# Optimization experiments

Hardware: AMD Instinct MI355X
Metric: run time of the kernel (lower is better)

## Reference

```python
import jax, jax.numpy as jnp
import numpy as np

HIDDEN = 64


def _lstm_cell(x, h, c, W_ih, W_hh, b_ih, b_hh):
    # gates: [B, 4*H], torch LSTMCell order: i, f, g, o
    gates = x @ W_ih.T + h @ W_hh.T + b_ih + b_hh
    i, f, g, o = jnp.split(gates, 4, axis=-1)
    i = jax.nn.sigmoid(i)
    f = jax.nn.sigmoid(f)
    g = jnp.tanh(g)
    o = jax.nn.sigmoid(o)
    c_new = f * c + i * g
    h_new = o * jnp.tanh(c_new)
    return h_new, c_new


def setup_inputs() -> dict:
    key = jax.random.key(0)
    ks = jax.random.split(key, 12)
    B, L, H = 1024, 512, HIDDEN
    k = 1.0 / np.sqrt(H)  # torch LSTMCell/Linear init scale
    u = lambda kk, shape: jax.random.uniform(kk, shape, jnp.float32, -k, k)
    return {
        "y": jax.random.normal(ks[0], (B, L), jnp.float32),
        "W_ih1": u(ks[1], (4 * H, 1)),
        "W_hh1": u(ks[2], (4 * H, H)),
        "b_ih1": u(ks[3], (4 * H,)),
        "b_hh1": u(ks[4], (4 * H,)),
        "W_ih2": u(ks[5], (4 * H, H)),
        "W_hh2": u(ks[6], (4 * H, H)),
        "b_ih2": u(ks[7], (4 * H,)),
        "b_hh2": u(ks[8], (4 * H,)),
        "W_lin": u(ks[9], (1, H)),
        "b_lin": u(ks[10], (1,)),
        "future_preds": 0,
    }


def reference(y, W_ih1, W_hh1, b_ih1, b_hh1, W_ih2, W_hh2, b_ih2, b_hh2,
              W_lin, b_lin, future_preds):
    B = y.shape[0]
    H = HIDDEN
    zeros = jnp.zeros((B, H), jnp.float32)

    def step(carry, x_t):
        h1, c1, h2, c2 = carry
        h1, c1 = _lstm_cell(x_t, h1, c1, W_ih1, W_hh1, b_ih1, b_hh1)
        h2, c2 = _lstm_cell(h1, h2, c2, W_ih2, W_hh2, b_ih2, b_hh2)
        out = h2 @ W_lin.T + b_lin  # [B, 1]
        return (h1, c1, h2, c2), out

    xs = y.T[:, :, None]  # [L, B, 1]
    carry, outs = jax.lax.scan(step, (zeros, zeros, zeros, zeros), xs)
    outputs = outs[:, :, 0].T  # [B, L]

    if future_preds > 0:
        def fstep(fc, _):
            h1, c1, h2, c2, out = fc
            h1, c1 = _lstm_cell(out, h1, c1, W_ih1, W_hh1, b_ih1, b_hh1)
            h2, c2 = _lstm_cell(h1, h2, c2, W_ih2, W_hh2, b_ih2, b_hh2)
            out = h2 @ W_lin.T + b_lin
            return (h1, c1, h2, c2, out), out
        last_out = outs[-1]  # [B, 1]
        _, fouts = jax.lax.scan(fstep, (*carry, last_out), None,
                                length=future_preds)
        outputs = jnp.concatenate([outputs, fouts[:, :, 0].T], axis=1)
    return outputs
```

## Files before the change

### kernel.cpp

```cpp
#include <hip/hip_runtime.h>
#include <math.h>

#define LSEQ 512

typedef float  f32x4  __attribute__((ext_vector_type(4)));
typedef short  bf16x8 __attribute__((ext_vector_type(8)));

union Frag { uint32_t u[4]; bf16x8 h; };

__device__ __forceinline__ float frcp(float x) { return __builtin_amdgcn_rcpf(x); }
__device__ __forceinline__ float sigm(float x) { return frcp(1.0f + exp2f(-1.442695041f * x)); }
__device__ __forceinline__ float tanh_fast(float x) {
    float e = exp2f(2.885390082f * x);
    return 1.0f - 2.0f * frcp(e + 1.0f);
}

__device__ __forceinline__ uint32_t pack_hi_u(uint32_t b0, uint32_t b1) {
    return __builtin_amdgcn_perm(b1, b0, 0x07060302u);
}

__device__ __forceinline__ void load_wfrag(const float* __restrict__ W, int sl, int nn, int g4,
                                           Frag fh[4][2], Frag fl[4][2]) {
#pragma unroll
    for (int gt = 0; gt < 4; ++gt) {
        const float* p = W + (size_t)(64 * gt + 16 * sl + nn) * 64 + g4 * 8;
#pragma unroll
        for (int kt = 0; kt < 2; ++kt) {
            float4 va = ((const float4*)(p + kt * 32))[0];
            float4 vb = ((const float4*)(p + kt * 32))[1];
            float v[8] = {va.x, va.y, va.z, va.w, vb.x, vb.y, vb.z, vb.w};
#pragma unroll
            for (int j = 0; j < 4; ++j) {
                uint32_t b0 = __float_as_uint(v[2 * j]);
                uint32_t b1 = __float_as_uint(v[2 * j + 1]);
                float l0 = v[2 * j]     - __uint_as_float(b0 & 0xffff0000u);
                float l1 = v[2 * j + 1] - __uint_as_float(b1 & 0xffff0000u);
                fh[gt][kt].u[j] = pack_hi_u(b0, b1);
                fl[gt][kt].u[j] = pack_hi_u(__float_as_uint(l0), __float_as_uint(l1));
            }
        }
    }
}

__device__ __forceinline__ int hidx(int m, int j) {
    return m * 64 + ((((j >> 3) ^ (m & 7)) << 3) | (j & 7));
}

__device__ __forceinline__ void loadA(const uint16_t* __restrict__ ph,
                                      const uint16_t* __restrict__ pl,
                                      int mm, int g4, bf16x8 ah[2], bf16x8 al[2]) {
#pragma unroll
    for (int kt = 0; kt < 2; ++kt) {
        const int off = mm * 64 + ((((kt << 2) + g4) ^ (mm & 7)) << 3);
        ah[kt] = *(const bf16x8*)(ph + off);
        al[kt] = *(const bf16x8*)(pl + off);
    }
}

__device__ __forceinline__ void split_store(uint16_t* ph, uint16_t* pl, int idx, float x) {
    uint32_t xb = __float_as_uint(x);
    ph[idx] = (uint16_t)(xb >> 16);
    float lo = x - __uint_as_float(xb & 0xffff0000u);
    pl[idx] = (uint16_t)(__float_as_uint(lo) >> 16);
}

#define MFMA3(acc, AH, AL, BH, BL)                                                  \
    acc = __builtin_amdgcn_mfma_f32_16x16x32_bf16((AH), (BH).h, acc, 0, 0, 0);      \
    acc = __builtin_amdgcn_mfma_f32_16x16x32_bf16((AH), (BL).h, acc, 0, 0, 0);      \
    acc = __builtin_amdgcn_mfma_f32_16x16x32_bf16((AL), (BH).h, acc, 0, 0, 0);

__global__ __launch_bounds__(512, 1)
void lstm2_pipe(const float* __restrict__ y,
                const float* __restrict__ W_ih1, const float* __restrict__ W_hh1,
                const float* __restrict__ b_ih1, const float* __restrict__ b_hh1,
                const float* __restrict__ W_ih2, const float* __restrict__ W_hh2,
                const float* __restrict__ b_ih2, const float* __restrict__ b_hh2,
                const float* __restrict__ W_lin, const float* __restrict__ b_lin,
                float* __restrict__ out)
{
    __shared__ __align__(16) float    y_s[LSEQ * 16];
    __shared__ __align__(16) uint16_t h1h[2][1024];
    __shared__ __align__(16) uint16_t h1l[2][1024];
    __shared__ __align__(16) uint16_t h2h[2][1024];
    __shared__ __align__(16) uint16_t h2l[2][1024];
    __shared__ __align__(16) float    outS[16 * 521];

    const int tid  = threadIdx.x;
    const int w    = tid >> 6;
    const int lane = tid & 63;
    const int nn   = lane & 15;
    const int g4   = lane >> 4;
    const int mq   = g4 << 2;
    const int bg0  = blockIdx.x << 4;

    {
        const int m = tid >> 5, seg = tid & 31;
        const float4* yp = (const float4*)(y + (size_t)(bg0 + m) * LSEQ) + seg * 4;
#pragma unroll
        for (int c = 0; c < 4; ++c) {
            float4 v = yp[c];
            int t0 = seg * 16 + c * 4;
            y_s[(t0 + 0) * 16 + m] = v.x;
            y_s[(t0 + 1) * 16 + m] = v.y;
            y_s[(t0 + 2) * 16 + m] = v.z;
            y_s[(t0 + 3) * 16 + m] = v.w;
        }
        if (tid < 256) {
            uint4 z = {0u, 0u, 0u, 0u};
            ((uint4*)h1h)[tid] = z;
            ((uint4*)h1l)[tid] = z;
            ((uint4*)h2h)[tid] = z;
            ((uint4*)h2l)[tid] = z;
        }
    }
    __syncthreads();

    if (w < 4) {
        Frag bh[4][2], bl[4][2];
        load_wfrag(W_hh1, w, nn, g4, bh, bl);
        float bs1_[4], wih1_[4];
#pragma unroll
        for (int gt = 0; gt < 4; ++gt) {
            int row = 64 * gt + 16 * w + nn;
            bs1_[gt]  = b_ih1[row] + b_hh1[row];
            wih1_[gt] = W_ih1[row];
        }
        const int jj = 16 * w + nn;
        float c1[4] = {0.f, 0.f, 0.f, 0.f};

        float wl[16];
        float blin = 0.f;
        if (w == 0) {
            blin = b_lin[0];
            const float4* wp = (const float4*)W_lin + g4 * 4;
#pragma unroll
            for (int i = 0; i < 4; ++i) {
                float4 v = wp[i];
                wl[4 * i + 0] = v.x; wl[4 * i + 1] = v.y;
                wl[4 * i + 2] = v.z; wl[4 * i + 3] = v.w;
            }
        }

#pragma unroll 1
        for (int t = 0; t <= LSEQ; ++t) {
            if (t < LSEQ) {
                bf16x8 ah[2], al[2];
                loadA(h1h[(t + 1) & 1], h1l[(t + 1) & 1], nn, g4, ah, al);
                f32x4 xq = *(const f32x4*)&y_s[t * 16 + mq];
                f32x4 ac0[4], ac1[4];
#pragma unroll
                for (int g = 0; g < 4; ++g)
#pragma unroll
                    for (int r = 0; r < 4; ++r) {
                        ac0[g][r] = bs1_[g] + wih1_[g] * xq[r];
                        ac1[g][r] = 0.f;
                    }
#pragma unroll
                for (int g = 0; g < 4; ++g) {
                    MFMA3(ac0[g], ah[0], al[0], bh[g][0], bl[g][0]);
                    MFMA3(ac1[g], ah[1], al[1], bh[g][1], bl[g][1]);
                }
#pragma unroll
                for (int r = 0; r < 4; ++r) {
                    float iv = sigm(ac0[0][r] + ac1[0][r]);
                    float fv = sigm(ac0[1][r] + ac1[1][r]);
                    float gv = tanh_fast(ac0[2][r] + ac1[2][r]);
                    float ov = sigm(ac0[3][r] + ac1[3][r]);
                    c1[r] = fmaf(fv, c1[r], iv * gv);
                    float h1n = ov * tanh_fast(c1[r]);
                    split_store(h1h[t & 1], h1l[t & 1], hidx(mq + r, jj), h1n);
                }
            }
            if (w == 0 && t >= 2) {
                const uint16_t* ph = h2h[t & 1];
                const uint16_t* pl = h2l[t & 1];
                const int m = lane & 15;
                float s = 0.f;
#pragma unroll
                for (int oo = 0; oo < 2; ++oo) {
                    const int oct = 2 * g4 + oo;
                    const int off = m * 64 + ((oct ^ (m & 7)) << 3);
                    bf16x8 hv = *(const bf16x8*)(ph + off);
                    bf16x8 lv = *(const bf16x8*)(pl + off);
#pragma unroll
                    for (int i = 0; i < 8; ++i) {
                        float val = __uint_as_float(((uint32_t)(uint16_t)hv[i]) << 16)
                                  + __uint_as_float(((uint32_t)(uint16_t)lv[i]) << 16);
                        s = fmaf(val, wl[oo * 8 + i], s);
                    }
                }
                s += __shfl_xor(s, 16);
                s += __shfl_xor(s, 32);
                if (lane < 16) outS[m * 521 + (t - 2)] = s + blin;
            }
            __syncthreads();
        }
        if (w == 0) {
            const uint16_t* ph = h2h[1];
            const uint16_t* pl = h2l[1];
            const int m = lane & 15;
            float s = 0.f;
#pragma unroll
            for (int oo = 0; oo < 2; ++oo) {
                const int oct = 2 * g4 + oo;
                const int off = m * 64 + ((oct ^ (m & 7)) << 3);
                bf16x8 hv = *(const bf16x8*)(ph + off);
                bf16x8 lv = *(const bf16x8*)(pl + off);
#pragma unroll
                for (int i = 0; i < 8; ++i) {
                    float val = __uint_as_float(((uint32_t)(uint16_t)hv[i]) << 16)
                              + __uint_as_float(((uint32_t)(uint16_t)lv[i]) << 16);
                    s = fmaf(val, wl[oo * 8 + i], s);
                }
            }
            s += __shfl_xor(s, 16);
            s += __shfl_xor(s, 32);
            if (lane < 16) outS[m * 521 + (LSEQ - 1)] = s + blin;
        }
    } else {
        const int v = w - 4;
        Frag bih[4][2], bil[4][2], bhh[4][2], bhl[4][2];
        load_wfrag(W_ih2, v, nn, g4, bih, bil);
        load_wfrag(W_hh2, v, nn, g4, bhh, bhl);
        float bs2_[4];
#pragma unroll
        for (int gt = 0; gt < 4; ++gt) {
            int row = 64 * gt + 16 * v + nn;
            bs2_[gt] = b_ih2[row] + b_hh2[row];
        }
        const int jj = 16 * v + nn;
        float c2[4] = {0.f, 0.f, 0.f, 0.f};

#pragma unroll 1
        for (int t = 0; t <= LSEQ; ++t) {
            if (t >= 1) {
                bf16x8 a2h_[2], a2l_[2], a3h_[2], a3l_[2];
                loadA(h1h[(t - 1) & 1], h1l[(t - 1) & 1], nn, g4, a2h_, a2l_);
                loadA(h2h[t & 1],       h2l[t & 1],       nn, g4, a3h_, a3l_);
                f32x4 aca[4], acb[4];
#pragma unroll
                for (int g = 0; g < 4; ++g)
#pragma unroll
                    for (int r = 0; r < 4; ++r) { aca[g][r] = bs2_[g]; acb[g][r] = 0.f; }
                __builtin_amdgcn_s_setprio(1);
#pragma unroll
                for (int kt = 0; kt < 2; ++kt)
#pragma unroll
                    for (int g = 0; g < 4; ++g) {
                        MFMA3(aca[g], a2h_[kt], a2l_[kt], bih[g][kt], bil[g][kt]);
                        MFMA3(acb[g], a3h_[kt], a3l_[kt], bhh[g][kt], bhl[g][kt]);
                    }
                __builtin_amdgcn_s_setprio(0);
#pragma unroll
                for (int r = 0; r < 4; ++r) {
                    float iv = sigm(aca[0][r] + acb[0][r]);
                    float fv = sigm(aca[1][r] + acb[1][r]);
                    float gv = tanh_fast(aca[2][r] + acb[2][r]);
                    float ov = sigm(aca[3][r] + acb[3][r]);
                    c2[r] = fmaf(fv, c2[r], iv * gv);
                    float h2n = ov * tanh_fast(c2[r]);
                    split_store(h2h[(t - 1) & 1], h2l[(t - 1) & 1], hidx(mq + r, jj), h2n);
                }
            }
            __syncthreads();
        }
    }

    __syncthreads();

    {
        const int m  = tid >> 5;
        const int t0 = (tid & 31) << 4;
        float* op = out + (size_t)(bg0 + m) * LSEQ + t0;
        const float* sp = outS + m * 521 + t0;
#pragma unroll
        for (int k2 = 0; k2 < 4; ++k2) {
            float4 vv = make_float4(sp[4 * k2 + 0], sp[4 * k2 + 1],
                                    sp[4 * k2 + 2], sp[4 * k2 + 3]);
            *(float4*)(op + 4 * k2) = vv;
        }
    }
}

extern "C" void kernel_launch(void* const* d_in, const int* in_sizes, int n_in,
                              void* d_out, int out_size, void* d_ws, size_t ws_size,
                              hipStream_t stream) {
    const float* y     = (const float*)d_in[0];
    const float* W_ih1 = (const float*)d_in[1];
    const float* W_hh1 = (const float*)d_in[2];
    const float* b_ih1 = (const float*)d_in[3];
    const float* b_hh1 = (const float*)d_in[4];
    const float* W_ih2 = (const float*)d_in[5];
    const float* W_hh2 = (const float*)d_in[6];
    const float* b_ih2 = (const float*)d_in[7];
    const float* b_hh2 = (const float*)d_in[8];
    const float* W_lin = (const float*)d_in[9];
    const float* b_lin = (const float*)d_in[10];
    float* out = (float*)d_out;

    lstm2_pipe<<<dim3(64), dim3(512), 0, stream>>>(
        y, W_ih1, W_hh1, b_ih1, b_hh1, W_ih2, W_hh2, b_ih2, b_hh2,
        W_lin, b_lin, out);
}
```

Before: 824.0 us.

## Rotate output projection across layer-1 waves and vectorize gate math

The per-step linear output projection, previously always done by wave 0, now rotates among the four layer-1 waves by timestep, so no single wave carries the extra work every step. Gate activations are rewritten as packed 4-wide vector operations so the compiler can use packed FP32 instructions. In layer 2 the recurrent h2 operand is loaded and multiplied first, before the h1 input. The rotation requires every layer-1 wave to hold W_lin and b_lin in registers, which raises register use.

```diff
diff --git a/kernel.cpp b/kernel.cpp
--- a/kernel.cpp
+++ b/kernel.cpp
@@ -9,10 +9,24 @@
 union Frag { uint32_t u[4]; bf16x8 h; };
 
 __device__ __forceinline__ float frcp(float x) { return __builtin_amdgcn_rcpf(x); }
-__device__ __forceinline__ float sigm(float x) { return frcp(1.0f + exp2f(-1.442695041f * x)); }
-__device__ __forceinline__ float tanh_fast(float x) {
-    float e = exp2f(2.885390082f * x);
-    return 1.0f - 2.0f * frcp(e + 1.0f);
+
+__device__ __forceinline__ f32x4 vexp2(f32x4 x) {
+    f32x4 r;
+    r.x = exp2f(x.x); r.y = exp2f(x.y); r.z = exp2f(x.z); r.w = exp2f(x.w);
+    return r;
+}
+__device__ __forceinline__ f32x4 vrcp(f32x4 x) {
+    f32x4 r;
+    r.x = frcp(x.x); r.y = frcp(x.y); r.z = frcp(x.z); r.w = frcp(x.w);
+    return r;
+}
+__device__ __forceinline__ f32x4 vsigm(f32x4 x) {
+    f32x4 e = vexp2(x * -1.442695041f);
+    return vrcp(e + 1.0f);
+}
+__device__ __forceinline__ f32x4 vtanh(f32x4 x) {
+    f32x4 e = vexp2(x * 2.885390082f);
+    return 1.0f - 2.0f * vrcp(e + 1.0f);
 }
 
 __device__ __forceinline__ uint32_t pack_hi_u(uint32_t b0, uint32_t b1) {
@@ -126,12 +140,11 @@
             wih1_[gt] = W_ih1[row];
         }
         const int jj = 16 * w + nn;
-        float c1[4] = {0.f, 0.f, 0.f, 0.f};
+        f32x4 c1v = {0.f, 0.f, 0.f, 0.f};
 
         float wl[16];
-        float blin = 0.f;
-        if (w == 0) {
-            blin = b_lin[0];
+        const float blin = b_lin[0];
+        {
             const float4* wp = (const float4*)W_lin + g4 * 4;
 #pragma unroll
             for (int i = 0; i < 4; ++i) {
@@ -149,29 +162,26 @@
                 f32x4 xq = *(const f32x4*)&y_s[t * 16 + mq];
                 f32x4 ac0[4], ac1[4];
 #pragma unroll
-                for (int g = 0; g < 4; ++g)
-#pragma unroll
-                    for (int r = 0; r < 4; ++r) {
-                        ac0[g][r] = bs1_[g] + wih1_[g] * xq[r];
-                        ac1[g][r] = 0.f;
-                    }
+                for (int g = 0; g < 4; ++g) {
+                    ac0[g] = xq * wih1_[g] + bs1_[g];
+                    ac1[g] = 0.f;
+                }
 #pragma unroll
                 for (int g = 0; g < 4; ++g) {
                     MFMA3(ac0[g], ah[0], al[0], bh[g][0], bl[g][0]);
                     MFMA3(ac1[g], ah[1], al[1], bh[g][1], bl[g][1]);
                 }
-#pragma unroll
-                for (int r = 0; r < 4; ++r) {
-                    float iv = sigm(ac0[0][r] + ac1[0][r]);
-                    float fv = sigm(ac0[1][r] + ac1[1][r]);
-                    float gv = tanh_fast(ac0[2][r] + ac1[2][r]);
-                    float ov = sigm(ac0[3][r] + ac1[3][r]);
-                    c1[r] = fmaf(fv, c1[r], iv * gv);
-                    float h1n = ov * tanh_fast(c1[r]);
-                    split_store(h1h[t & 1], h1l[t & 1], hidx(mq + r, jj), h1n);
-                }
-            }
-            if (w == 0 && t >= 2) {
+                f32x4 gi = vsigm(ac0[0] + ac1[0]);
+                f32x4 gf = vsigm(ac0[1] + ac1[1]);
+                f32x4 gg = vtanh(ac0[2] + ac1[2]);
+                f32x4 go = vsigm(ac0[3] + ac1[3]);
+                c1v = gf * c1v + gi * gg;
+                f32x4 h1v = go * vtanh(c1v);
+#pragma unroll
+                for (int r = 0; r < 4; ++r)
+                    split_store(h1h[t & 1], h1l[t & 1], hidx(mq + r, jj), h1v[r]);
+            }
+            if (t >= 2 && w == ((t - 2) & 3)) {
                 const uint16_t* ph = h2h[t & 1];
                 const uint16_t* pl = h2l[t & 1];
                 const int m = lane & 15;
@@ -229,38 +239,35 @@
             bs2_[gt] = b_ih2[row] + b_hh2[row];
         }
         const int jj = 16 * v + nn;
-        float c2[4] = {0.f, 0.f, 0.f, 0.f};
+        f32x4 c2v = {0.f, 0.f, 0.f, 0.f};
 
 #pragma unroll 1
         for (int t = 0; t <= LSEQ; ++t) {
             if (t >= 1) {
-                bf16x8 a2h_[2], a2l_[2], a3h_[2], a3l_[2];
+                bf16x8 a3h_[2], a3l_[2], a2h_[2], a2l_[2];
+                loadA(h2h[t & 1],       h2l[t & 1],       nn, g4, a3h_, a3l_);
                 loadA(h1h[(t - 1) & 1], h1l[(t - 1) & 1], nn, g4, a2h_, a2l_);
-                loadA(h2h[t & 1],       h2l[t & 1],       nn, g4, a3h_, a3l_);
                 f32x4 aca[4], acb[4];
 #pragma unroll
-                for (int g = 0; g < 4; ++g)
-#pragma unroll
-                    for (int r = 0; r < 4; ++r) { aca[g][r] = bs2_[g]; acb[g][r] = 0.f; }
+                for (int g = 0; g < 4; ++g) { acb[g] = bs2_[g]; aca[g] = 0.f; }
                 __builtin_amdgcn_s_setprio(1);
 #pragma unroll
                 for (int kt = 0; kt < 2; ++kt)
 #pragma unroll
                     for (int g = 0; g < 4; ++g) {
+                        MFMA3(acb[g], a3h_[kt], a3l_[kt], bhh[g][kt], bhl[g][kt]);
                         MFMA3(aca[g], a2h_[kt], a2l_[kt], bih[g][kt], bil[g][kt]);
-                        MFMA3(acb[g], a3h_[kt], a3l_[kt], bhh[g][kt], bhl[g][kt]);
                     }
                 __builtin_amdgcn_s_setprio(0);
-#pragma unroll
-                for (int r = 0; r < 4; ++r) {
-                    float iv = sigm(aca[0][r] + acb[0][r]);
-                    float fv = sigm(aca[1][r] + acb[1][r]);
-                    float gv = tanh_fast(aca[2][r] + acb[2][r]);
-                    float ov = sigm(aca[3][r] + acb[3][r]);
-                    c2[r] = fmaf(fv, c2[r], iv * gv);
-                    float h2n = ov * tanh_fast(c2[r]);
-                    split_store(h2h[(t - 1) & 1], h2l[(t - 1) & 1], hidx(mq + r, jj), h2n);
-                }
+                f32x4 gi = vsigm(aca[0] + acb[0]);
+                f32x4 gf = vsigm(aca[1] + acb[1]);
+                f32x4 gg = vtanh(aca[2] + acb[2]);
+                f32x4 go = vsigm(aca[3] + acb[3]);
+                c2v = gf * c2v + gi * gg;
+                f32x4 h2v = go * vtanh(c2v);
+#pragma unroll
+                for (int r = 0; r < 4; ++r)
+                    split_store(h2h[(t - 1) & 1], h2l[(t - 1) & 1], hidx(mq + r, jj), h2v[r]);
             }
             __syncthreads();
         }
```

Result: no change. 826.6 us (+0.3%).
